# Kernel optimization log

Measured on AMD Instinct MI355X. Metric: run time of the kernel, lower is better.

## Reference

```python
import jax, jax.numpy as jnp
import numpy as np

N_NODES = 100000
N_EDGES = 1600000
N_GRAPHS = 2048
D = 128
H = 128
EPS = 1e-5


def gcn_conv(x, src, dst, W, b, n):
    # x: [N, Din], W: [Din, Dout]; GCN with added self-loops and symmetric norm
    xw = x @ W                                       # [N, Dout]
    deg = jnp.zeros((n,), x.dtype).at[dst].add(1.0) + 1.0  # deg of A+I (counted on dst)
    dinv = jax.lax.rsqrt(deg)                        # [N]
    norm = dinv[src] * dinv[dst]                     # [E]
    msg = xw[src] * norm[:, None]                    # [E, Dout] gather + scale
    agg = jax.ops.segment_sum(msg, dst, num_segments=n)
    agg = agg + xw * (dinv * dinv)[:, None]          # self-loop contribution
    return agg + b


def gru_step_h0(x, W_ih, W_hh, b_ih, b_hh):
    # single GRU step with h0 = 0 (PyTorch gate order r, z, n)
    h0 = jnp.zeros_like(x)
    gi = x @ W_ih.T + b_ih                           # [G, 3H]
    gh = h0 @ W_hh.T + b_hh                          # [G, 3H] (zeros + b_hh)
    ir, iz, inn = jnp.split(gi, 3, axis=-1)
    hr, hz, hn = jnp.split(gh, 3, axis=-1)
    r = jax.nn.sigmoid(ir + hr)
    z = jax.nn.sigmoid(iz + hz)
    n = jnp.tanh(inn + r * hn)
    return (1.0 - z) * n + z * h0


def setup_inputs() -> dict:
    key = jax.random.key(0)
    ks = jax.random.split(key, 10)
    x = jax.random.normal(ks[0], (N_NODES, D), jnp.float32)
    edge_index = jax.random.randint(ks[1], (2, N_EDGES), 0, N_NODES, jnp.int32)
    batch = jnp.sort(jax.random.randint(ks[2], (N_NODES,), 0, N_GRAPHS, jnp.int32))
    s = 1.0 / np.sqrt(H)
    return {
        "x": x,
        "edge_index": edge_index,
        "batch": batch,
        "W1": jax.random.normal(ks[3], (D, H), jnp.float32) * s,
        "b1": jnp.zeros((H,), jnp.float32),
        "W2": jax.random.normal(ks[4], (H, H), jnp.float32) * s,
        "b2": jnp.zeros((H,), jnp.float32),
        "W_ih": jax.random.normal(ks[5], (3 * H, H), jnp.float32) * s,
        "W_hh": jax.random.normal(ks[6], (3 * H, H), jnp.float32) * s,
        "b_ih": jnp.zeros((3 * H,), jnp.float32),
        "b_hh": jnp.zeros((3 * H,), jnp.float32),
        "W_lin": jax.random.normal(ks[7], (1, H), jnp.float32) * s,
        "b_lin": jnp.zeros((1,), jnp.float32),
    }


def reference(x, edge_index, batch, W1, b1, W2, b2, W_ih, W_hh, b_ih, b_hh, W_lin, b_lin):
    src, dst = edge_index[0], edge_index[1]
    n = x.shape[0]
    h = jax.nn.relu(gcn_conv(x, src, dst, W1, b1, n))
    h = gcn_conv(h, src, dst, W2, b2, n)
    # global_mean_pool over graph ids
    sums = jax.ops.segment_sum(h, batch, num_segments=N_GRAPHS)
    cnts = jax.ops.segment_sum(jnp.ones((n,), h.dtype), batch, num_segments=N_GRAPHS)
    g = sums / jnp.maximum(cnts, 1.0)[:, None]       # [G, H]
    # dropout p=0.5 in eval mode -> identity
    g = gru_step_h0(g, W_ih, W_hh, b_ih, b_hh)
    g = jax.nn.relu(g)
    mu = jnp.mean(g, axis=-1, keepdims=True)
    var = jnp.mean(jnp.square(g - mu), axis=-1, keepdims=True)
    g = (g - mu) * jax.lax.rsqrt(var + EPS)          # layer_norm, no affine
    return g @ W_lin.T + b_lin                       # [G, 1]
```

## Files before the change

### kernel.cpp

```cpp
#include <hip/hip_runtime.h>
#include <hip/hip_bf16.h>
#include <math.h>

#define DHID 128
#define SH 8
#define BIN_T 8192
#define CAPSH 13
#define SRC_SH 13

typedef __attribute__((ext_vector_type(8))) short bf16x8;
typedef __attribute__((ext_vector_type(4))) float f32x4;

__device__ __forceinline__ int atomAddI(int* p, int v) {
    return __hip_atomic_fetch_add(p, v, __ATOMIC_RELAXED, __HIP_MEMORY_SCOPE_AGENT);
}
__device__ __forceinline__ float bf_lo(unsigned u) { return __uint_as_float(u << 16); }
__device__ __forceinline__ float bf_hi(unsigned u) { return __uint_as_float(u & 0xffff0000u); }
__device__ __forceinline__ float bf_us(unsigned short u) { return __uint_as_float((unsigned)u << 16); }
__device__ __forceinline__ unsigned short bf16_1(float f) {
    unsigned u = __float_as_uint(f);
    u += 0x7fffu + ((u >> 16) & 1u);
    return (unsigned short)(u >> 16);
}
__device__ __forceinline__ unsigned pack_bf16x2(float a, float b) {
    unsigned ua = __float_as_uint(a);
    unsigned ub = __float_as_uint(b);
    ua = (ua + 0x7fffu + ((ua >> 16) & 1u)) >> 16;
    ub = (ub + 0x7fffu + ((ub >> 16) & 1u)) & 0xffff0000u;
    return ua | ub;
}

__global__ __launch_bounds__(256) void bin_edges(const int* __restrict__ src,
                                                 const int* __restrict__ dst,
                                                 int* __restrict__ bcur,
                                                 unsigned* __restrict__ staged,
                                                 const float* __restrict__ W1,
                                                 const float* __restrict__ W2,
                                                 const float* __restrict__ Wih,
                                                 unsigned short* __restrict__ Wt1,
                                                 unsigned short* __restrict__ Wt2,
                                                 unsigned short* __restrict__ Wihb,
                                                 int E, int NB, int nb_bin) {
    int t = threadIdx.x;
    if (blockIdx.x >= nb_bin) {
        int idx = (blockIdx.x - nb_bin) * 256 + t;
        if (idx < 16384) {
            int k = idx >> 7, n = idx & 127;
            Wt1[n * 128 + k] = bf16_1(W1[idx]);
        } else if (idx < 32768) {
            int j = idx - 16384;
            int k = j >> 7, n = j & 127;
            Wt2[n * 128 + k] = bf16_1(W2[j]);
        } else if (idx < 32768 + 49152) {
            int j = idx - 32768;
            Wihb[j] = bf16_1(Wih[j]);
        }
        return;
    }
    __shared__ int lh[512], lbase[512], lcur[512];
    int e0 = blockIdx.x * BIN_T;
    int eend = min(e0 + BIN_T, E);
    for (int i = t; i < NB; i += 256) { lh[i] = 0; lcur[i] = 0; }
    __syncthreads();
    for (int e = e0 + t; e < eend; e += 256)
        atomicAdd(&lh[dst[e] >> SH], 1);
    __syncthreads();
    for (int i = t; i < NB; i += 256)
        lbase[i] = lh[i] ? atomAddI(&bcur[i], lh[i]) : 0;
    __syncthreads();
    for (int e = e0 + t; e < eend; e += 256) {
        int d = dst[e];
        int b = d >> SH;
        int pos = lbase[b] + atomicAdd(&lcur[b], 1);
        staged[((size_t)b << CAPSH) + pos] =
            (unsigned)src[e] | ((unsigned)(d & ((1 << SH) - 1)) << 24);
    }
}

__global__ __launch_bounds__(256) void scatter_gemm(const unsigned* __restrict__ staged,
                                                    const int* __restrict__ bcur,
                                                    int* __restrict__ off,
                                                    float* __restrict__ dinv,
                                                    int* __restrict__ rec,
                                                    int N, int E, int NB,
                                                    const float* __restrict__ Xf,
                                                    const unsigned short* __restrict__ Wt,
                                                    unsigned short* __restrict__ Y) {
    __shared__ __align__(16) unsigned char smem[52224];
    const int tid = threadIdx.x;
    if (blockIdx.x < NB) {
        int* hist = (int*)smem;
        int* sh   = (int*)(smem + 16384);
        int t = tid;
        int b = blockIdx.x;
        int node0 = b << SH;

        int s0 = (t < b) ? bcur[t] : 0;
        int s1 = (256 + t < b) ? bcur[256 + t] : 0;
        int s = s0 + s1;
#pragma unroll
        for (int o = 1; o < 64; o <<= 1) s += __shfl_xor(s, o);
        if ((t & 63) == 0) sh[t >> 6] = s;
        __syncthreads();
        int base = sh[0] + sh[1] + sh[2] + sh[3];
        __syncthreads();

        for (int i = t; i < 4096; i += 256) hist[i] = 0;
        __syncthreads();
        int cnt_b = bcur[b];
        const unsigned* st = staged + ((size_t)b << CAPSH);
        for (int j = t; j < cnt_b; j += 256) {
            unsigned w = st[j];
            int key = (int)((w >> 24) << 4) | (int)((w & 0xFFFFFFu) >> SRC_SH);
            atomicAdd(&hist[key], 1);
        }
        __syncthreads();

        int loc[16];
        int run = 0;
        int base16 = t * 16;
#pragma unroll
        for (int i = 0; i < 16; i++) { loc[i] = run; run += hist[base16 + i]; }
        sh[t] = run;
        __syncthreads();
#pragma unroll
        for (int o = 1; o < 256; o <<= 1) {
            int x = (t >= o) ? sh[t - o] : 0;
            __syncthreads();
            sh[t] += x;
            __syncthreads();
        }
        int excl = sh[t] - run;
#pragma unroll
        for (int i = 0; i < 16; i++) hist[base16 + i] = base + excl + loc[i];

        int node = node0 + t;
        if (node < N) {
            off[node] = base + excl;
            dinv[node] = rsqrtf((float)run + 1.0f);
        }
        if (b == NB - 1 && t == 0) off[N] = E;
        __syncthreads();

        for (int j = t; j < cnt_b; j += 256) {
            unsigned w = st[j];
            int key = (int)((w >> 24) << 4) | (int)((w & 0xFFFFFFu) >> SRC_SH);
            int pos = atomicAdd(&hist[key], 1);
            rec[pos] = (int)(w & 0xFFFFFFu);
        }
    } else {
        unsigned short* Xs = (unsigned short*)smem;
        unsigned short* Ws = (unsigned short*)(smem + 17408);
        {
            const uint4* W4 = (const uint4*)Wt;
#pragma unroll
            for (int i = 0; i < 8; i++) {
                int idx = tid + i * 256;
                int r = idx >> 4, c8 = idx & 15;
                *(uint4*)&Ws[r * 136 + c8 * 8] = W4[idx];
            }
        }
        const int row0 = (blockIdx.x - NB) * 64;
        {
            const float4* X4 = (const float4*)Xf;
#pragma unroll
            for (int i = 0; i < 8; i++) {
                int idx = tid + i * 256;
                int r = idx >> 5, c4 = idx & 31;
                float4 v = make_float4(0.f, 0.f, 0.f, 0.f);
                if (row0 + r < N) v = X4[(size_t)(row0 + r) * 32 + c4];
                uint2 pk = make_uint2(pack_bf16x2(v.x, v.y), pack_bf16x2(v.z, v.w));
                *(uint2*)&Xs[r * 136 + c4 * 4] = pk;
            }
        }
        __syncthreads();

        const int lane = tid & 63;
        const int wv = tid >> 6;
        const int m = lane & 15, quad = lane >> 4;
        const int wrow = wv * 16;

        f32x4 acc[8];
#pragma unroll
        for (int i = 0; i < 8; i++) acc[i] = (f32x4){0.f, 0.f, 0.f, 0.f};

#pragma unroll
        for (int kc = 0; kc < 4; kc++) {
            bf16x8 a = *(const bf16x8*)&Xs[(wrow + m) * 136 + kc * 32 + quad * 8];
#pragma unroll
            for (int nt = 0; nt < 8; nt++) {
                bf16x8 bfr = *(const bf16x8*)&Ws[(nt * 16 + m) * 136 + kc * 32 + quad * 8];
                acc[nt] = __builtin_amdgcn_mfma_f32_16x16x32_bf16(a, bfr, acc[nt], 0, 0, 0);
            }
        }

#pragma unroll
        for (int r = 0; r < 4; r++) {
            int lrow = wrow + quad * 4 + r;
#pragma unroll
            for (int nt = 0; nt < 8; nt++)
                Xs[lrow * 136 + nt * 16 + m] = bf16_1(acc[nt][r]);
        }
        __syncthreads();
#pragma unroll
        for (int i = 0; i < 4; i++) {
            int idx = tid + i * 256;
            int r = idx >> 4, c8 = idx & 15;
            if (row0 + r < N)
                *(uint4*)&Y[(size_t)(row0 + r) * DHID + c8 * 8] =
                    *(const uint4*)&Xs[r * 136 + c8 * 8];
        }
    }
}

__global__ __launch_bounds__(256) void aggregate(const unsigned short* __restrict__ A,
                                                 const float* __restrict__ dinv,
                                                 const int* __restrict__ off,
                                                 const int* __restrict__ rec,
                                                 const float* __restrict__ bias,
                                                 unsigned short* __restrict__ Bout,
                                                 int N, int mode) {
    int node = blockIdx.x * 4 + (threadIdx.x >> 6);
    if (node >= N) return;
    int lane = threadIdx.x & 63;
    int q  = lane >> 4;
    int ql = lane & 15;
    float di = dinv[node];
    float2 acc[4];
    if (q == 0) {
        float s = di * di;
        uint4 v = ((const uint4*)(A + (size_t)node * DHID))[ql];
        const float4* bb = (const float4*)(bias + ql * 8);
        float4 b0 = bb[0], b1 = bb[1];
        acc[0] = make_float2(bf_lo(v.x) * s + b0.x, bf_hi(v.x) * s + b0.y);
        acc[1] = make_float2(bf_lo(v.y) * s + b0.z, bf_hi(v.y) * s + b0.w);
        acc[2] = make_float2(bf_lo(v.z) * s + b1.x, bf_hi(v.z) * s + b1.y);
        acc[3] = make_float2(bf_lo(v.w) * s + b1.z, bf_hi(v.w) * s + b1.w);
    } else {
#pragma unroll
        for (int i = 0; i < 4; i++) acc[i] = make_float2(0.f, 0.f);
    }
    int j = off[node] + q;
    int jend = off[node + 1];
    if (j + 4 < jend) {
        int s0 = rec[j], s1 = rec[j + 4];
        for (; j + 12 < jend; j += 8) {
            int n0 = rec[j + 8], n1 = rec[j + 12];
            uint4 v0 = ((const uint4*)(A + (size_t)s0 * DHID))[ql];
            uint4 v1 = ((const uint4*)(A + (size_t)s1 * DHID))[ql];
            float w0 = dinv[s0] * di;
            float w1 = dinv[s1] * di;
            acc[0].x += bf_lo(v0.x) * w0 + bf_lo(v1.x) * w1;
            acc[0].y += bf_hi(v0.x) * w0 + bf_hi(v1.x) * w1;
            acc[1].x += bf_lo(v0.y) * w0 + bf_lo(v1.y) * w1;
            acc[1].y += bf_hi(v0.y) * w0 + bf_hi(v1.y) * w1;
            acc[2].x += bf_lo(v0.z) * w0 + bf_lo(v1.z) * w1;
            acc[2].y += bf_hi(v0.z) * w0 + bf_hi(v1.z) * w1;
            acc[3].x += bf_lo(v0.w) * w0 + bf_lo(v1.w) * w1;
            acc[3].y += bf_hi(v0.w) * w0 + bf_hi(v1.w) * w1;
            s0 = n0; s1 = n1;
        }
        {
            uint4 v0 = ((const uint4*)(A + (size_t)s0 * DHID))[ql];
            uint4 v1 = ((const uint4*)(A + (size_t)s1 * DHID))[ql];
            float w0 = dinv[s0] * di;
            float w1 = dinv[s1] * di;
            acc[0].x += bf_lo(v0.x) * w0 + bf_lo(v1.x) * w1;
            acc[0].y += bf_hi(v0.x) * w0 + bf_hi(v1.x) * w1;
            acc[1].x += bf_lo(v0.y) * w0 + bf_lo(v1.y) * w1;
            acc[1].y += bf_hi(v0.y) * w0 + bf_hi(v1.y) * w1;
            acc[2].x += bf_lo(v0.z) * w0 + bf_lo(v1.z) * w1;
            acc[2].y += bf_hi(v0.z) * w0 + bf_hi(v1.z) * w1;
            acc[3].x += bf_lo(v0.w) * w0 + bf_lo(v1.w) * w1;
            acc[3].y += bf_hi(v0.w) * w0 + bf_hi(v1.w) * w1;
            j += 8;
        }
    }
    if (j < jend) {
        int s0 = rec[j];
        uint4 v0 = ((const uint4*)(A + (size_t)s0 * DHID))[ql];
        float w0 = dinv[s0] * di;
        acc[0].x += bf_lo(v0.x) * w0;
        acc[0].y += bf_hi(v0.x) * w0;
        acc[1].x += bf_lo(v0.y) * w0;
        acc[1].y += bf_hi(v0.y) * w0;
        acc[2].x += bf_lo(v0.z) * w0;
        acc[2].y += bf_hi(v0.z) * w0;
        acc[3].x += bf_lo(v0.w) * w0;
        acc[3].y += bf_hi(v0.w) * w0;
    }
#pragma unroll
    for (int i = 0; i < 4; i++) {
        acc[i].x += __shfl_xor(acc[i].x, 16);
        acc[i].y += __shfl_xor(acc[i].y, 16);
        acc[i].x += __shfl_xor(acc[i].x, 32);
        acc[i].y += __shfl_xor(acc[i].y, 32);
    }
    if (q == 0) {
        if (mode == 1) {
#pragma unroll
            for (int i = 0; i < 4; i++) {
                acc[i].x = fmaxf(acc[i].x, 0.f);
                acc[i].y = fmaxf(acc[i].y, 0.f);
            }
        }
        uint4 pk;
        pk.x = pack_bf16x2(acc[0].x, acc[0].y);
        pk.y = pack_bf16x2(acc[1].x, acc[1].y);
        pk.z = pack_bf16x2(acc[2].x, acc[2].y);
        pk.w = pack_bf16x2(acc[3].x, acc[3].y);
        ((uint4*)(Bout + (size_t)node * DHID))[ql] = pk;
    }
}

__global__ __launch_bounds__(256) void gemm_mfma(const void* __restrict__ Xv,
                                                 const unsigned short* __restrict__ Wt,
                                                 unsigned short* __restrict__ Y,
                                                 int N, int x_is_bf16,
                                                 int wstride, int ystride) {
    __shared__ unsigned short Xs[64 * 136];
    __shared__ unsigned short Ws[128 * 136];
    const int tid = threadIdx.x;
    const unsigned short* Wg = Wt + (size_t)blockIdx.y * wstride;
    unsigned short* Yg = Y + (size_t)blockIdx.y * ystride;

    {
        const uint4* W4 = (const uint4*)Wg;
#pragma unroll
        for (int i = 0; i < 8; i++) {
            int idx = tid + i * 256;
            int r = idx >> 4, c8 = idx & 15;
            *(uint4*)&Ws[r * 136 + c8 * 8] = W4[idx];
        }
    }
    const int row0 = blockIdx.x * 64;
    if (x_is_bf16) {
        const uint4* X4 = (const uint4*)Xv;
#pragma unroll
        for (int i = 0; i < 4; i++) {
            int idx = tid + i * 256;
            int r = idx >> 4, c8 = idx & 15;
            uint4 v = make_uint4(0u, 0u, 0u, 0u);
            if (row0 + r < N) v = X4[(size_t)(row0 + r) * 16 + c8];
            *(uint4*)&Xs[r * 136 + c8 * 8] = v;
        }
    } else {
        const float4* X4 = (const float4*)Xv;
#pragma unroll
        for (int i = 0; i < 8; i++) {
            int idx = tid + i * 256;
            int r = idx >> 5, c4 = idx & 31;
            float4 v = make_float4(0.f, 0.f, 0.f, 0.f);
            if (row0 + r < N) v = X4[(size_t)(row0 + r) * 32 + c4];
            uint2 pk = make_uint2(pack_bf16x2(v.x, v.y), pack_bf16x2(v.z, v.w));
            *(uint2*)&Xs[r * 136 + c4 * 4] = pk;
        }
    }
    __syncthreads();

    const int lane = tid & 63;
    const int wv = tid >> 6;
    const int m = lane & 15, quad = lane >> 4;
    const int wrow = wv * 16;

    f32x4 acc[8];
#pragma unroll
    for (int i = 0; i < 8; i++) acc[i] = (f32x4){0.f, 0.f, 0.f, 0.f};

#pragma unroll
    for (int kc = 0; kc < 4; kc++) {
        bf16x8 a = *(const bf16x8*)&Xs[(wrow + m) * 136 + kc * 32 + quad * 8];
#pragma unroll
        for (int nt = 0; nt < 8; nt++) {
            bf16x8 b = *(const bf16x8*)&Ws[(nt * 16 + m) * 136 + kc * 32 + quad * 8];
            acc[nt] = __builtin_amdgcn_mfma_f32_16x16x32_bf16(a, b, acc[nt], 0, 0, 0);
        }
    }

#pragma unroll
    for (int r = 0; r < 4; r++) {
        int lrow = wrow + quad * 4 + r;
#pragma unroll
        for (int nt = 0; nt < 8; nt++)
            Xs[lrow * 136 + nt * 16 + m] = bf16_1(acc[nt][r]);
    }
    __syncthreads();
#pragma unroll
    for (int i = 0; i < 4; i++) {
        int idx = tid + i * 256;
        int r = idx >> 4, c8 = idx & 15;
        if (row0 + r < N)
            *(uint4*)&Yg[(size_t)(row0 + r) * DHID + c8 * 8] =
                *(const uint4*)&Xs[r * 136 + c8 * 8];
    }
}

__global__ __launch_bounds__(256) void tail_head(const unsigned short* __restrict__ B,
                                                 const int* __restrict__ batch,
                                                 const unsigned short* __restrict__ Wihb,
                                                 const float* __restrict__ b_ih,
                                                 const float* __restrict__ b_hh,
                                                 const float* __restrict__ W_lin,
                                                 const float* __restrict__ b_lin,
                                                 float* __restrict__ out,
                                                 int N, int G) {
    __shared__ float grow[128];
    __shared__ float psum[4][128];
    __shared__ float gi[384];
    __shared__ float red[4];
    __shared__ int se[2];
    const int t = threadIdx.x;
    const int g = blockIdx.x;
    if (t < 2) {
        int target = g + t, lo = 0, hi = N;
        while (lo < hi) {
            int mid = (lo + hi) >> 1;
            if (batch[mid] < target) lo = mid + 1; else hi = mid;
        }
        se[t] = lo;
    }
    __syncthreads();
    const int s = se[0], e = se[1];

    const int c2 = t & 63;
    const int rh = t >> 6;
    float sx = 0.f, sy = 0.f;
    for (int r = s + rh; r < e; r += 4) {
        unsigned u = *(const unsigned*)(B + (size_t)r * DHID + c2 * 2);
        sx += bf_lo(u);
        sy += bf_hi(u);
    }
    *(float2*)&psum[rh][c2 * 2] = make_float2(sx, sy);
    __syncthreads();
    if (t < 128) {
        grow[t] = (psum[0][t] + psum[1][t] + psum[2][t] + psum[3][t]) /
                  fmaxf((float)(e - s), 1.0f);
    }
    __syncthreads();

    {
        float a0 = 0.f;
        const uint4* wr = (const uint4*)(Wihb + (size_t)t * DHID);
#pragma unroll
        for (int k8 = 0; k8 < 16; k8++) {
            uint4 wv = wr[k8];
            const float* gk = &grow[k8 * 8];
            a0 += bf_lo(wv.x) * gk[0] + bf_hi(wv.x) * gk[1]
                + bf_lo(wv.y) * gk[2] + bf_hi(wv.y) * gk[3]
                + bf_lo(wv.z) * gk[4] + bf_hi(wv.z) * gk[5]
                + bf_lo(wv.w) * gk[6] + bf_hi(wv.w) * gk[7];
        }
        gi[t] = a0;
    }
    if (t < 128) {
        float a1 = 0.f;
        const uint4* wr = (const uint4*)(Wihb + (size_t)(256 + t) * DHID);
#pragma unroll
        for (int k8 = 0; k8 < 16; k8++) {
            uint4 wv = wr[k8];
            const float* gk = &grow[k8 * 8];
            a1 += bf_lo(wv.x) * gk[0] + bf_hi(wv.x) * gk[1]
                + bf_lo(wv.y) * gk[2] + bf_hi(wv.y) * gk[3]
                + bf_lo(wv.z) * gk[4] + bf_hi(wv.z) * gk[5]
                + bf_lo(wv.w) * gk[6] + bf_hi(wv.w) * gk[7];
        }
        gi[256 + t] = a1;
    }
    __syncthreads();

    float y = 0.f, wl = 0.f;
    if (t < 128) {
        float d0 = gi[t], d1 = gi[128 + t], d2 = gi[256 + t];
        float rg = 1.f / (1.f + expf(-(d0 + b_ih[t] + b_hh[t])));
        float zg = 1.f / (1.f + expf(-(d1 + b_ih[128 + t] + b_hh[128 + t])));
        float ng = tanhf(d2 + b_ih[256 + t] + rg * b_hh[256 + t]);
        y = fmaxf((1.f - zg) * ng, 0.f);
        wl = W_lin[t];
    }
    auto blockSum = [&](float v) -> float {
#pragma unroll
        for (int o = 1; o < 64; o <<= 1) v += __shfl_xor(v, o);
        __syncthreads();
        if ((t & 63) == 0) red[t >> 6] = v;
        __syncthreads();
        return red[0] + red[1] + red[2] + red[3];
    };
    float mu = blockSum(y) * (1.f / 128.f);
    float dy = (t < 128) ? (y - mu) : 0.f;
    float var = blockSum(dy * dy) * (1.f / 128.f);
    float yn = dy * rsqrtf(var + 1e-5f);
    float tot = blockSum(yn * wl);
    if (t == 0) out[g] = tot + b_lin[0];
}

extern "C" void kernel_launch(void* const* d_in, const int* in_sizes, int n_in,
                              void* d_out, int out_size, void* d_ws, size_t ws_size,
                              hipStream_t stream) {
    const float* x     = (const float*)d_in[0];
    const int*   ei    = (const int*)d_in[1];
    const int*   batch = (const int*)d_in[2];
    const float* W1    = (const float*)d_in[3];
    const float* b1    = (const float*)d_in[4];
    const float* W2    = (const float*)d_in[5];
    const float* b2    = (const float*)d_in[6];
    const float* W_ih  = (const float*)d_in[7];
    const float* b_ih  = (const float*)d_in[9];
    const float* b_hh  = (const float*)d_in[10];
    const float* W_lin = (const float*)d_in[11];
    const float* b_lin = (const float*)d_in[12];
    float* out = (float*)d_out;

    const int N = in_sizes[0] / DHID;
    const int E = in_sizes[1] / 2;
    const int G = out_size;
    const int* src = ei;
    const int* dst = ei + E;
    const int NB = (N + (1 << SH) - 1) >> SH;

    auto align256 = [](size_t v) { return (v + 255) & ~(size_t)255; };
    char* p = (char*)d_ws;
    size_t used = 0;
    auto carve = [&](size_t bytes) -> char* {
        char* q = p + used;
        used += align256(bytes);
        return q;
    };

    int*   off    = (int*)carve(((size_t)N + 1) * 4);
    int*   bcur   = (int*)carve(512 * 4);
    float* dinv   = (float*)carve((size_t)N * 4);
    unsigned* staged = (unsigned*)carve(((size_t)NB << CAPSH) * 4);
    int*   rec    = (int*)carve((size_t)E * 4);
    unsigned short* Wt1  = (unsigned short*)carve((size_t)128 * 128 * 2);
    unsigned short* Wt2  = (unsigned short*)carve((size_t)128 * 128 * 2);
    unsigned short* Wihb = (unsigned short*)carve((size_t)3 * 128 * 128 * 2);
    unsigned short* A    = (unsigned short*)carve((size_t)N * DHID * 2);
    unsigned short* B1b  = (unsigned short*)carve((size_t)N * DHID * 2);
    size_t matB = (size_t)N * DHID * 2;
    unsigned short* B2b;
    if (ws_size >= used + matB) {
        B2b = (unsigned short*)carve(matB);
    } else {
        B2b = (unsigned short*)d_in[0];
    }

    dim3 blk(256);
    int nb_g  = (N + 63) / 64;
    int nb_ag = (N + 3) / 4;
    int nb_bin = (E + BIN_T - 1) / BIN_T;
    int nb_wp  = (81920 + 255) / 256;

    hipMemsetAsync(bcur, 0, (size_t)NB * 4, stream);
    bin_edges<<<nb_bin + nb_wp, blk, 0, stream>>>(src, dst, bcur, staged,
                                                  W1, W2, W_ih, Wt1, Wt2, Wihb,
                                                  E, NB, nb_bin);
    scatter_gemm<<<NB + nb_g, blk, 0, stream>>>(staged, bcur, off, dinv, rec,
                                                N, E, NB, x, Wt1, A);

    aggregate<<<nb_ag, blk, 0, stream>>>(A, dinv, off, rec, b1, B1b, N, 1);

    gemm_mfma<<<dim3(nb_g, 1), blk, 0, stream>>>(B1b, Wt2, A, N, 1, 0, 0);
    aggregate<<<nb_ag, blk, 0, stream>>>(A, dinv, off, rec, b2, B2b, N, 0);

    tail_head<<<G, blk, 0, stream>>>(B2b, batch, Wihb, b_ih, b_hh, W_lin, b_lin,
                                     out, N, G);
}
```

Measured before the change: 341.0 us.

## Fuse aggregate, GEMM, aggregate and tail into one cooperative persistent kernel

Replaces four separate launches (aggregate, gemm_mfma, aggregate, tail_head) with a single cooperative persistent kernel that uses grid-wide syncs between phases. The second GEMM now reads weight fragments straight from global memory instead of staging them in LDS. The aim is to remove launch gaps and tail effects between the short kernels. In exchange it adds grid.sync barriers and caps occupancy at six blocks per CU, and the global weight reads may be slower than LDS reads.

```diff
diff --git a/kernel.cpp b/kernel.cpp
--- a/kernel.cpp
+++ b/kernel.cpp
@@ -1,6 +1,9 @@
 #include <hip/hip_runtime.h>
+#include <hip/hip_cooperative_groups.h>
 #include <hip/hip_bf16.h>
 #include <math.h>
+
+namespace cg = cooperative_groups;
 
 #define DHID 128
 #define SH 8
@@ -213,16 +216,13 @@
     }
 }
 
-__global__ __launch_bounds__(256) void aggregate(const unsigned short* __restrict__ A,
-                                                 const float* __restrict__ dinv,
-                                                 const int* __restrict__ off,
-                                                 const int* __restrict__ rec,
-                                                 const float* __restrict__ bias,
-                                                 unsigned short* __restrict__ Bout,
-                                                 int N, int mode) {
-    int node = blockIdx.x * 4 + (threadIdx.x >> 6);
-    if (node >= N) return;
-    int lane = threadIdx.x & 63;
+__device__ __forceinline__ void agg_node(const unsigned short* __restrict__ A,
+                                         const float* __restrict__ dinv,
+                                         const int* __restrict__ off,
+                                         const int* __restrict__ rec,
+                                         const float* __restrict__ bias,
+                                         unsigned short* __restrict__ Bout,
+                                         int node, int lane, int relu) {
     int q  = lane >> 4;
     int ql = lane & 15;
     float di = dinv[node];
@@ -297,7 +297,7 @@
         acc[i].y += __shfl_xor(acc[i].y, 32);
     }
     if (q == 0) {
-        if (mode == 1) {
+        if (relu) {
 #pragma unroll
             for (int i = 0; i < 4; i++) {
                 acc[i].x = fmaxf(acc[i].x, 0.f);
@@ -313,70 +313,37 @@
     }
 }
 
-__global__ __launch_bounds__(256) void gemm_mfma(const void* __restrict__ Xv,
-                                                 const unsigned short* __restrict__ Wt,
-                                                 unsigned short* __restrict__ Y,
-                                                 int N, int x_is_bf16,
-                                                 int wstride, int ystride) {
-    __shared__ unsigned short Xs[64 * 136];
-    __shared__ unsigned short Ws[128 * 136];
-    const int tid = threadIdx.x;
-    const unsigned short* Wg = Wt + (size_t)blockIdx.y * wstride;
-    unsigned short* Yg = Y + (size_t)blockIdx.y * ystride;
-
-    {
-        const uint4* W4 = (const uint4*)Wg;
-#pragma unroll
-        for (int i = 0; i < 8; i++) {
-            int idx = tid + i * 256;
-            int r = idx >> 4, c8 = idx & 15;
-            *(uint4*)&Ws[r * 136 + c8 * 8] = W4[idx];
-        }
-    }
-    const int row0 = blockIdx.x * 64;
-    if (x_is_bf16) {
-        const uint4* X4 = (const uint4*)Xv;
-#pragma unroll
-        for (int i = 0; i < 4; i++) {
-            int idx = tid + i * 256;
-            int r = idx >> 4, c8 = idx & 15;
-            uint4 v = make_uint4(0u, 0u, 0u, 0u);
-            if (row0 + r < N) v = X4[(size_t)(row0 + r) * 16 + c8];
-            *(uint4*)&Xs[r * 136 + c8 * 8] = v;
-        }
-    } else {
-        const float4* X4 = (const float4*)Xv;
-#pragma unroll
-        for (int i = 0; i < 8; i++) {
-            int idx = tid + i * 256;
-            int r = idx >> 5, c4 = idx & 31;
-            float4 v = make_float4(0.f, 0.f, 0.f, 0.f);
-            if (row0 + r < N) v = X4[(size_t)(row0 + r) * 32 + c4];
-            uint2 pk = make_uint2(pack_bf16x2(v.x, v.y), pack_bf16x2(v.z, v.w));
-            *(uint2*)&Xs[r * 136 + c4 * 4] = pk;
-        }
-    }
-    __syncthreads();
-
+__device__ __forceinline__ void gemm_tile_wg(const unsigned short* __restrict__ X,
+                                             const unsigned short* __restrict__ Wt,
+                                             unsigned short* __restrict__ Y,
+                                             int N, int row0,
+                                             unsigned short* Xs, int tid) {
+    const uint4* X4 = (const uint4*)X;
+#pragma unroll
+    for (int i = 0; i < 4; i++) {
+        int idx = tid + i * 256;
+        int r = idx >> 4, c8 = idx & 15;
+        uint4 v = make_uint4(0u, 0u, 0u, 0u);
+        if (row0 + r < N) v = X4[(size_t)(row0 + r) * 16 + c8];
+        *(uint4*)&Xs[r * 136 + c8 * 8] = v;
+    }
+    __syncthreads();
     const int lane = tid & 63;
     const int wv = tid >> 6;
     const int m = lane & 15, quad = lane >> 4;
     const int wrow = wv * 16;
-
     f32x4 acc[8];
 #pragma unroll
     for (int i = 0; i < 8; i++) acc[i] = (f32x4){0.f, 0.f, 0.f, 0.f};
-
 #pragma unroll
     for (int kc = 0; kc < 4; kc++) {
-        bf16x8 a = *(const bf16x8*)&Xs[(wrow + m) * 136 + kc * 32 + quad * 8];
+        bf16x8 av = *(const bf16x8*)&Xs[(wrow + m) * 136 + kc * 32 + quad * 8];
 #pragma unroll
         for (int nt = 0; nt < 8; nt++) {
-            bf16x8 b = *(const bf16x8*)&Ws[(nt * 16 + m) * 136 + kc * 32 + quad * 8];
-            acc[nt] = __builtin_amdgcn_mfma_f32_16x16x32_bf16(a, b, acc[nt], 0, 0, 0);
-        }
-    }
-
+            bf16x8 bv = *(const bf16x8*)(Wt + (nt * 16 + m) * 128 + kc * 32 + quad * 8);
+            acc[nt] = __builtin_amdgcn_mfma_f32_16x16x32_bf16(av, bv, acc[nt], 0, 0, 0);
+        }
+    }
 #pragma unroll
     for (int r = 0; r < 4; r++) {
         int lrow = wrow + quad * 4 + r;
@@ -390,37 +357,40 @@
         int idx = tid + i * 256;
         int r = idx >> 4, c8 = idx & 15;
         if (row0 + r < N)
-            *(uint4*)&Yg[(size_t)(row0 + r) * DHID + c8 * 8] =
+            *(uint4*)&Y[(size_t)(row0 + r) * DHID + c8 * 8] =
                 *(const uint4*)&Xs[r * 136 + c8 * 8];
     }
-}
-
-__global__ __launch_bounds__(256) void tail_head(const unsigned short* __restrict__ B,
-                                                 const int* __restrict__ batch,
-                                                 const unsigned short* __restrict__ Wihb,
-                                                 const float* __restrict__ b_ih,
-                                                 const float* __restrict__ b_hh,
-                                                 const float* __restrict__ W_lin,
-                                                 const float* __restrict__ b_lin,
-                                                 float* __restrict__ out,
-                                                 int N, int G) {
-    __shared__ float grow[128];
-    __shared__ float psum[4][128];
-    __shared__ float gi[384];
-    __shared__ float red[4];
-    __shared__ int se[2];
-    const int t = threadIdx.x;
-    const int g = blockIdx.x;
+    __syncthreads();
+}
+
+struct TailSmem {
+    float grow[128];
+    float psum[4][128];
+    float gi[384];
+    float red[4];
+    int se[2];
+};
+
+__device__ __forceinline__ void tail_one(const unsigned short* __restrict__ B,
+                                         const int* __restrict__ batch,
+                                         const unsigned short* __restrict__ Wihb,
+                                         const float* __restrict__ b_ih,
+                                         const float* __restrict__ b_hh,
+                                         const float* __restrict__ W_lin,
+                                         const float* __restrict__ b_lin,
+                                         float* __restrict__ out,
+                                         int N, int g, TailSmem* S, int t) {
+    __syncthreads();
     if (t < 2) {
         int target = g + t, lo = 0, hi = N;
         while (lo < hi) {
             int mid = (lo + hi) >> 1;
             if (batch[mid] < target) lo = mid + 1; else hi = mid;
         }
-        se[t] = lo;
-    }
-    __syncthreads();
-    const int s = se[0], e = se[1];
+        S->se[t] = lo;
+    }
+    __syncthreads();
+    const int s = S->se[0], e = S->se[1];
 
     const int c2 = t & 63;
     const int rh = t >> 6;
@@ -430,11 +400,11 @@
         sx += bf_lo(u);
         sy += bf_hi(u);
     }
-    *(float2*)&psum[rh][c2 * 2] = make_float2(sx, sy);
+    *(float2*)&S->psum[rh][c2 * 2] = make_float2(sx, sy);
     __syncthreads();
     if (t < 128) {
-        grow[t] = (psum[0][t] + psum[1][t] + psum[2][t] + psum[3][t]) /
-                  fmaxf((float)(e - s), 1.0f);
+        S->grow[t] = (S->psum[0][t] + S->psum[1][t] + S->psum[2][t] + S->psum[3][t]) /
+                     fmaxf((float)(e - s), 1.0f);
     }
     __syncthreads();
 
@@ -444,13 +414,13 @@
 #pragma unroll
         for (int k8 = 0; k8 < 16; k8++) {
             uint4 wv = wr[k8];
-            const float* gk = &grow[k8 * 8];
+            const float* gk = &S->grow[k8 * 8];
             a0 += bf_lo(wv.x) * gk[0] + bf_hi(wv.x) * gk[1]
                 + bf_lo(wv.y) * gk[2] + bf_hi(wv.y) * gk[3]
                 + bf_lo(wv.z) * gk[4] + bf_hi(wv.z) * gk[5]
                 + bf_lo(wv.w) * gk[6] + bf_hi(wv.w) * gk[7];
         }
-        gi[t] = a0;
+        S->gi[t] = a0;
     }
     if (t < 128) {
         float a1 = 0.f;
@@ -458,19 +428,19 @@
 #pragma unroll
         for (int k8 = 0; k8 < 16; k8++) {
             uint4 wv = wr[k8];
-            const float* gk = &grow[k8 * 8];
+            const float* gk = &S->grow[k8 * 8];
             a1 += bf_lo(wv.x) * gk[0] + bf_hi(wv.x) * gk[1]
                 + bf_lo(wv.y) * gk[2] + bf_hi(wv.y) * gk[3]
                 + bf_lo(wv.z) * gk[4] + bf_hi(wv.z) * gk[5]
                 + bf_lo(wv.w) * gk[6] + bf_hi(wv.w) * gk[7];
         }
-        gi[256 + t] = a1;
+        S->gi[256 + t] = a1;
     }
     __syncthreads();
 
     float y = 0.f, wl = 0.f;
     if (t < 128) {
-        float d0 = gi[t], d1 = gi[128 + t], d2 = gi[256 + t];
+        float d0 = S->gi[t], d1 = S->gi[128 + t], d2 = S->gi[256 + t];
         float rg = 1.f / (1.f + expf(-(d0 + b_ih[t] + b_hh[t])));
         float zg = 1.f / (1.f + expf(-(d1 + b_ih[128 + t] + b_hh[128 + t])));
         float ng = tanhf(d2 + b_ih[256 + t] + rg * b_hh[256 + t]);
@@ -481,9 +451,9 @@
 #pragma unroll
         for (int o = 1; o < 64; o <<= 1) v += __shfl_xor(v, o);
         __syncthreads();
-        if ((t & 63) == 0) red[t >> 6] = v;
-        __syncthreads();
-        return red[0] + red[1] + red[2] + red[3];
+        if ((t & 63) == 0) S->red[t >> 6] = v;
+        __syncthreads();
+        return S->red[0] + S->red[1] + S->red[2] + S->red[3];
     };
     float mu = blockSum(y) * (1.f / 128.f);
     float dy = (t < 128) ? (y - mu) : 0.f;
@@ -491,6 +461,61 @@
     float yn = dy * rsqrtf(var + 1e-5f);
     float tot = blockSum(yn * wl);
     if (t == 0) out[g] = tot + b_lin[0];
+}
+
+struct MegaArgs {
+    unsigned short* A;
+    const float* dinv;
+    const int* off;
+    const int* rec;
+    const float* b1;
+    const float* b2;
+    unsigned short* B1b;
+    const unsigned short* Wt2;
+    unsigned short* B2b;
+    const int* batch;
+    const unsigned short* Wihb;
+    const float* b_ih;
+    const float* b_hh;
+    const float* W_lin;
+    const float* b_lin;
+    float* out;
+    int N, G, nag, ntile;
+};
+
+__global__ __launch_bounds__(256, 6) void mega(MegaArgs a) {
+    cg::grid_group grid = cg::this_grid();
+    __shared__ __align__(16) unsigned char smem[17408];
+    const int tid = threadIdx.x;
+    const int lane = tid & 63;
+
+    for (int grp = blockIdx.x; grp < a.nag; grp += gridDim.x) {
+        int node = grp * 4 + (tid >> 6);
+        if (node < a.N)
+            agg_node(a.A, a.dinv, a.off, a.rec, a.b1, a.B1b, node, lane, 1);
+    }
+    grid.sync();
+
+    {
+        unsigned short* Xs = (unsigned short*)smem;
+        for (int tile = blockIdx.x; tile < a.ntile; tile += gridDim.x)
+            gemm_tile_wg(a.B1b, a.Wt2, a.A, a.N, tile * 64, Xs, tid);
+    }
+    grid.sync();
+
+    for (int grp = blockIdx.x; grp < a.nag; grp += gridDim.x) {
+        int node = grp * 4 + (tid >> 6);
+        if (node < a.N)
+            agg_node(a.A, a.dinv, a.off, a.rec, a.b2, a.B2b, node, lane, 0);
+    }
+    grid.sync();
+
+    {
+        TailSmem* ts = (TailSmem*)smem;
+        for (int g = blockIdx.x; g < a.G; g += gridDim.x)
+            tail_one(a.B2b, a.batch, a.Wihb, a.b_ih, a.b_hh, a.W_lin, a.b_lin,
+                     a.out, a.N, g, ts, tid);
+    }
 }
 
 extern "C" void kernel_launch(void* const* d_in, const int* in_sizes, int n_in,
@@ -546,7 +571,6 @@
 
     dim3 blk(256);
     int nb_g  = (N + 63) / 64;
-    int nb_ag = (N + 3) / 4;
     int nb_bin = (E + BIN_T - 1) / BIN_T;
     int nb_wp  = (81920 + 255) / 256;
 
@@ -557,11 +581,19 @@
     scatter_gemm<<<NB + nb_g, blk, 0, stream>>>(staged, bcur, off, dinv, rec,
                                                 N, E, NB, x, Wt1, A);
 
-    aggregate<<<nb_ag, blk, 0, stream>>>(A, dinv, off, rec, b1, B1b, N, 1);
-
-    gemm_mfma<<<dim3(nb_g, 1), blk, 0, stream>>>(B1b, Wt2, A, N, 1, 0, 0);
-    aggregate<<<nb_ag, blk, 0, stream>>>(A, dinv, off, rec, b2, B2b, N, 0);
-
-    tail_head<<<G, blk, 0, stream>>>(B2b, batch, Wihb, b_ih, b_hh, W_lin, b_lin,
-                                     out, N, G);
-}
+    MegaArgs ma;
+    ma.A = A;       ma.dinv = dinv;   ma.off = off;     ma.rec = rec;
+    ma.b1 = b1;     ma.b2 = b2;       ma.B1b = B1b;     ma.Wt2 = Wt2;
+    ma.B2b = B2b;   ma.batch = batch; ma.Wihb = Wihb;   ma.b_ih = b_ih;
+    ma.b_hh = b_hh; ma.W_lin = W_lin; ma.b_lin = b_lin; ma.out = out;
+    ma.N = N;       ma.G = G;         ma.nag = (N + 3) / 4;  ma.ntile = nb_g;
+
+    int maxPerCU = 0;
+    hipOccupancyMaxActiveBlocksPerMultiprocessor(&maxPerCU, mega, 256, 0);
+    if (maxPerCU <= 0) maxPerCU = 4;
+    int perCU = maxPerCU < 6 ? maxPerCU : 6;
+    int nblk = perCU * 256;
+
+    void* kargs[] = { (void*)&ma };
+    hipLaunchCooperativeKernel((const void*)mega, dim3(nblk), blk, kargs, 0, stream);
+}
```

Result: slower. 868.2 us (+154.6%).

## Halve dst bucket size and shrink edge bin tiles for more parallel blocks

Applied to the files above, without the earlier changes.

Destination buckets drop from 256 to 128 nodes and edge bin tiles from 8192 to 2048 edges. This roughly doubles the number of scatter/CSR-build blocks and quadruples the binning blocks, to spread the preprocessing work across more CUs. The binning kernel now loads each thread's 8 src/dst pairs into registers once instead of reading dst twice. The scatter prefix sum and the bcur and shared-memory sizes are adjusted to the new bucket count. The trade-off is more global atomics on bcur and less work per block.

```diff
diff --git a/kernel.cpp b/kernel.cpp
--- a/kernel.cpp
+++ b/kernel.cpp
@@ -3,9 +3,9 @@
 #include <math.h>
 
 #define DHID 128
-#define SH 8
-#define BIN_T 8192
-#define CAPSH 13
+#define SH 7
+#define BIN_T 2048
+#define CAPSH 12
 #define SRC_SH 13
 
 typedef __attribute__((ext_vector_type(8))) short bf16x8;
@@ -57,23 +57,34 @@
         }
         return;
     }
-    __shared__ int lh[512], lbase[512], lcur[512];
+    __shared__ int lh[1024], lbase[1024], lcur[1024];
     int e0 = blockIdx.x * BIN_T;
     int eend = min(e0 + BIN_T, E);
     for (int i = t; i < NB; i += 256) { lh[i] = 0; lcur[i] = 0; }
     __syncthreads();
-    for (int e = e0 + t; e < eend; e += 256)
-        atomicAdd(&lh[dst[e] >> SH], 1);
+    int sv[8], dv[8];
+#pragma unroll
+    for (int i = 0; i < 8; i++) {
+        int e = e0 + t + i * 256;
+        if (e < eend) { sv[i] = src[e]; dv[i] = dst[e]; }
+        else { sv[i] = 0; dv[i] = -1; }
+    }
+#pragma unroll
+    for (int i = 0; i < 8; i++)
+        if (dv[i] >= 0) atomicAdd(&lh[dv[i] >> SH], 1);
     __syncthreads();
     for (int i = t; i < NB; i += 256)
         lbase[i] = lh[i] ? atomAddI(&bcur[i], lh[i]) : 0;
     __syncthreads();
-    for (int e = e0 + t; e < eend; e += 256) {
-        int d = dst[e];
-        int b = d >> SH;
-        int pos = lbase[b] + atomicAdd(&lcur[b], 1);
-        staged[((size_t)b << CAPSH) + pos] =
-            (unsigned)src[e] | ((unsigned)(d & ((1 << SH) - 1)) << 24);
+#pragma unroll
+    for (int i = 0; i < 8; i++) {
+        if (dv[i] >= 0) {
+            int d = dv[i];
+            int b = d >> SH;
+            int pos = lbase[b] + atomicAdd(&lcur[b], 1);
+            staged[((size_t)b << CAPSH) + pos] =
+                (unsigned)sv[i] | ((unsigned)(d & ((1 << SH) - 1)) << 24);
+        }
     }
 }
 
@@ -90,14 +101,16 @@
     const int tid = threadIdx.x;
     if (blockIdx.x < NB) {
         int* hist = (int*)smem;
-        int* sh   = (int*)(smem + 16384);
+        int* sh   = (int*)(smem + 8192);
         int t = tid;
         int b = blockIdx.x;
         int node0 = b << SH;
 
         int s0 = (t < b) ? bcur[t] : 0;
         int s1 = (256 + t < b) ? bcur[256 + t] : 0;
-        int s = s0 + s1;
+        int s2 = (512 + t < b) ? bcur[512 + t] : 0;
+        int s3 = (768 + t < b) ? bcur[768 + t] : 0;
+        int s = s0 + s1 + s2 + s3;
 #pragma unroll
         for (int o = 1; o < 64; o <<= 1) s += __shfl_xor(s, o);
         if ((t & 63) == 0) sh[t >> 6] = s;
@@ -105,7 +118,7 @@
         int base = sh[0] + sh[1] + sh[2] + sh[3];
         __syncthreads();
 
-        for (int i = t; i < 4096; i += 256) hist[i] = 0;
+        for (int i = t; i < 2048; i += 256) hist[i] = 0;
         __syncthreads();
         int cnt_b = bcur[b];
         const unsigned* st = staged + ((size_t)b << CAPSH);
@@ -118,10 +131,12 @@
 
         int loc[16];
         int run = 0;
-        int base16 = t * 16;
-#pragma unroll
-        for (int i = 0; i < 16; i++) { loc[i] = run; run += hist[base16 + i]; }
-        sh[t] = run;
+        if (t < 128) {
+            int base16 = t * 16;
+#pragma unroll
+            for (int i = 0; i < 16; i++) { loc[i] = run; run += hist[base16 + i]; }
+        }
+        sh[t] = (t < 128) ? run : 0;
         __syncthreads();
 #pragma unroll
         for (int o = 1; o < 256; o <<= 1) {
@@ -131,13 +146,15 @@
             __syncthreads();
         }
         int excl = sh[t] - run;
-#pragma unroll
-        for (int i = 0; i < 16; i++) hist[base16 + i] = base + excl + loc[i];
-
-        int node = node0 + t;
-        if (node < N) {
-            off[node] = base + excl;
-            dinv[node] = rsqrtf((float)run + 1.0f);
+        if (t < 128) {
+            int base16 = t * 16;
+#pragma unroll
+            for (int i = 0; i < 16; i++) hist[base16 + i] = base + excl + loc[i];
+            int node = node0 + t;
+            if (node < N) {
+                off[node] = base + excl;
+                dinv[node] = rsqrtf((float)run + 1.0f);
+            }
         }
         if (b == NB - 1 && t == 0) off[N] = E;
         __syncthreads();
@@ -527,7 +544,7 @@
     };
 
     int*   off    = (int*)carve(((size_t)N + 1) * 4);
-    int*   bcur   = (int*)carve(512 * 4);
+    int*   bcur   = (int*)carve(1024 * 4);
     float* dinv   = (float*)carve((size_t)N * 4);
     unsigned* staged = (unsigned*)carve(((size_t)NB << CAPSH) * 4);
     int*   rec    = (int*)carve((size_t)E * 4);
@@ -550,7 +567,7 @@
     int nb_bin = (E + BIN_T - 1) / BIN_T;
     int nb_wp  = (81920 + 255) / 256;
 
-    hipMemsetAsync(bcur, 0, (size_t)NB * 4, stream);
+    hipMemsetAsync(bcur, 0, 1024 * 4, stream);
     bin_edges<<<nb_bin + nb_wp, blk, 0, stream>>>(src, dst, bcur, staged,
                                                   W1, W2, W_ih, Wt1, Wt2, Wihb,
                                                   E, NB, nb_bin);
```

After: 339.8 us. No clear change (-0.4%).
